# Performance work log

Hardware: AMD Instinct MI355X
Metric: run time of the kernel (lower is better)

## Reference

```python
import jax, jax.numpy as jnp
import numpy as np

NUM_NODES = 50000
NUM_EDGES = 800000
HIDDEN = 128
HEADS = 8
HEAD_DIM = HIDDEN // HEADS  # 16
FF_HIDDEN = 4 * HIDDEN
LN_EPS = 1e-5


def _xavier(key, shape, gain=0.01):
    fan_out, fan_in = shape
    bound = gain * np.sqrt(6.0 / (fan_in + fan_out))
    return jax.random.uniform(key, shape, jnp.float32, -bound, bound)


def setup_inputs() -> dict:
    key = jax.random.key(0)
    ks = jax.random.split(key, 10)
    x = jax.random.normal(ks[0], (NUM_NODES, HIDDEN), jnp.float32)
    edge_index = jax.random.randint(ks[1], (2, NUM_EDGES), 0, NUM_NODES, jnp.int64)
    return {
        "x": x,
        "edge_index": edge_index,
        "Wq": _xavier(ks[2], (HIDDEN, HIDDEN)),
        "bq": jnp.zeros((HIDDEN,), jnp.float32),
        "Wk": _xavier(ks[3], (HIDDEN, HIDDEN)),
        "bk": jnp.zeros((HIDDEN,), jnp.float32),
        "Wv": _xavier(ks[4], (HIDDEN, HIDDEN)),
        "bv": jnp.zeros((HIDDEN,), jnp.float32),
        "Wo": _xavier(ks[5], (HIDDEN, HIDDEN)),
        "bo": jnp.zeros((HIDDEN,), jnp.float32),
        "W1": _xavier(ks[6], (FF_HIDDEN, HIDDEN)),
        "b1": jnp.zeros((FF_HIDDEN,), jnp.float32),
        "W2": _xavier(ks[7], (HIDDEN, FF_HIDDEN)),
        "b2": jnp.zeros((HIDDEN,), jnp.float32),
        "g1": jnp.ones((HIDDEN,), jnp.float32),
        "be1": jnp.zeros((HIDDEN,), jnp.float32),
        "g2": jnp.ones((HIDDEN,), jnp.float32),
        "be2": jnp.zeros((HIDDEN,), jnp.float32),
    }


def _layernorm(v, g, b):
    mu = jnp.mean(v, axis=-1, keepdims=True)
    var = jnp.mean(jnp.square(v - mu), axis=-1, keepdims=True)
    return (v - mu) * jax.lax.rsqrt(var + LN_EPS) * g + b


def _forward(x, edge_index, Wq, bq, Wk, bk, Wv, bv, Wo, bo, W1, b1, W2, b2, g1, be1, g2, be2):
    src = edge_index[0]  # key/value side (_j)
    dst = edge_index[1]  # query side (_i), aggregation index
    scale = 1.0 / np.sqrt(HEAD_DIM)

    # Euclidean manifold: GeometricLinear == plain linear
    q = (x @ Wq.T + bq).reshape(NUM_NODES, HEADS, HEAD_DIM)
    k = (x @ Wk.T + bk).reshape(NUM_NODES, HEADS, HEAD_DIM)
    v = (x @ Wv.T + bv).reshape(NUM_NODES, HEADS, HEAD_DIM)

    # per-edge attention scores [E, H]
    alpha = jnp.einsum('ehd,ehd->eh', q[dst], k[src]) * scale
    # segment softmax over destination nodes
    m = jax.ops.segment_max(alpha, dst, num_segments=NUM_NODES)  # [N, H]
    ea = jnp.exp(alpha - m[dst])
    denom = jax.ops.segment_sum(ea, dst, num_segments=NUM_NODES)  # [N, H]
    alpha = ea / (denom[dst] + 1e-16)

    # scatter-add weighted values -> [N, H, D]
    agg = jax.ops.segment_sum(v[src] * alpha[..., None], dst, num_segments=NUM_NODES)
    att = agg.reshape(NUM_NODES, HIDDEN) @ Wo.T + bo

    # residual + norm1 (Euclidean)
    h = _layernorm(x + att, g1, be1)

    # feed-forward: fc1 -> exact GELU -> fc2
    ff = (jax.nn.gelu(h @ W1.T + b1, approximate=False)) @ W2.T + b2

    # residual + norm2
    return _layernorm(h + ff, g2, be2)


def reference(x, edge_index, Wq, bq, Wk, bk, Wv, bv, Wo, bo, W1, b1, W2, b2, g1, be1, g2, be2):
    return _forward(x, edge_index, Wq, bq, Wk, bk, Wv, bv, Wo, bo, W1, b1, W2, b2, g1, be1, g2, be2)
```

## Files before the change

kernel.cpp:

```cpp
#include <hip/hip_runtime.h>
#include <math.h>

#define N_HEADS 8
#define HEAD_DIM 16
#define HID 128
#define QKV_ROWB 512

typedef unsigned short ushort_t;
typedef __attribute__((ext_vector_type(8))) short short8;
typedef __attribute__((ext_vector_type(4))) float floatx4;
typedef __attribute__((ext_vector_type(2))) float f32x2;

#define KV_SCALE 64.0f
#define KV_INV_SCALE 0.015625f

__device__ __forceinline__ ushort_t f2bf(float f) {
    unsigned u = __float_as_uint(f);
    unsigned r = (u + 0x7FFFu + ((u >> 16) & 1u)) >> 16;
    return (ushort_t)r;
}
__device__ __forceinline__ float bf2f(ushort_t u) {
    return __uint_as_float(((unsigned)u) << 16);
}

__device__ __forceinline__ void gld_lds16(const void* g, void* l) {
    __builtin_amdgcn_global_load_lds(
        (const __attribute__((address_space(1))) void*)g,
        (__attribute__((address_space(3))) void*)l, 16, 0, 0);
}

__device__ __forceinline__ float gelu_f(float x) {
    float z = fabsf(x) * 0.70710678118654752f;
    float t = 1.0f / (1.0f + 0.3275911f * z);
    float y = t * (0.254829592f + t * (-0.284496736f + t * (1.421413741f
            + t * (-1.453152027f + t * 1.061405429f))));
    float e = 1.0f - y * __expf(-z * z);
    e = copysignf(e, x);
    return 0.5f * x * (1.0f + e);
}

__global__ __launch_bounds__(256)
void prep_kernel(const float* __restrict__ x,
                 const float* __restrict__ Wq, const float* __restrict__ Wk,
                 const float* __restrict__ Wv, const float* __restrict__ Wo,
                 const float* __restrict__ W1, const float* __restrict__ W2,
                 const float* __restrict__ bq, const float* __restrict__ bk,
                 const float* __restrict__ bv,
                 const int* __restrict__ dst, int* __restrict__ cnt, int E,
                 ushort_t* __restrict__ xb, ushort_t* __restrict__ wts,
                 float* __restrict__ bqkv, int xpairs)
{
    int i = blockIdx.x * 256 + threadIdx.x;
    if (i < xpairs) {
        float2 v = ((const float2*)x)[i];
        xb[i * 2]     = f2bf(v.x);
        xb[i * 2 + 1] = f2bf(v.y);
        return;
    }
    int j = i - xpairs;
    if (j < 98304) {
        const float* s; int off;
        if (j < 32768) {
            if (j < 8192)       { s = Wq; off = j; }
            else if (j < 16384) { s = Wk; off = j - 8192; }
            else if (j < 24576) { s = Wv; off = j - 16384; }
            else                { s = Wo; off = j - 24576; }
        } else if (j < 65536)   { s = W1; off = j - 32768; }
        else                    { s = W2; off = j - 65536; }
        float2 v = ((const float2*)s)[off];
        wts[j * 2]     = f2bf(v.x);
        wts[j * 2 + 1] = f2bf(v.y);
        return;
    }
    int b = j - 98304;
    if (b < 384) {
        bqkv[b] = (b < 128) ? bq[b] : (b < 256) ? bk[b - 128] : bv[b - 256];
        return;
    }
    int e = b - 384;
    if (e < E) atomicAdd(&cnt[dst[e]], 1);
}

template<int MT, int ACT, int LN, int OUTF>
__global__ __launch_bounds__(256)
void gemm_t(const ushort_t* __restrict__ A, int lda, int M,
            const ushort_t* __restrict__ W, int K,
            const float* __restrict__ bias,
            float* __restrict__ outf, ushort_t* __restrict__ outb, int ostride,
            const float* __restrict__ resf, const ushort_t* __restrict__ resb,
            const float* __restrict__ g, const float* __restrict__ be)
{
    constexpr int MI   = MT / 32;
    constexpr int HALF = MT * 64 + 128 * 64;
    constexpr int BNC  = MT * 136;
    constexpr int SB   = (2 * HALF > BNC) ? 2 * HALF : BNC;
    __shared__ __align__(16) ushort_t sbuf[SB];
    __shared__ float pS[LN ? MT : 1][2];
    __shared__ float pQ[LN ? MT : 1][2];

    const int tid  = threadIdx.x;
    const int wave = tid >> 6, lane = tid & 63;
    const int gm0 = blockIdx.x * MT;
    const int o0  = blockIdx.y * 128;
    const int mhalf = wave >> 1, ohalf = wave & 1;

    auto stage = [&](int kc, int h) {
        ushort_t* As = sbuf + h * HALF;
        ushort_t* Ws = As + MT * 64;
#pragma unroll
        for (int it = 0; it < 4; ++it) {
            int s   = it * 256 + tid;
            int ln  = s & 63;
            int grp = s >> 6;
            int tile = grp >> 1, kst = grp & 1;
            int row = tile * 16 + (ln & 15);
            int kk  = kst * 32 + (ln >> 4) * 8;
            gld_lds16(&W[(size_t)(o0 + row) * K + kc + kk],
                      &Ws[(it * 256 + wave * 64) * 8]);
        }
#pragma unroll
        for (int it = 0; it < MT / 32; ++it) {
            int s   = it * 256 + tid;
            int ln  = s & 63;
            int grp = s >> 6;
            int tile = grp >> 1, kst = grp & 1;
            int row = tile * 16 + (ln & 15);
            int kk  = kst * 32 + (ln >> 4) * 8;
            int ar = gm0 + row; if (ar >= M) ar = M - 1;
            gld_lds16(&A[(size_t)ar * lda + kc + kk],
                      &As[(it * 256 + wave * 64) * 8]);
        }
    };

    floatx4 acc[MI][4];
#pragma unroll
    for (int i = 0; i < MI; ++i)
#pragma unroll
        for (int j = 0; j < 4; ++j) acc[i][j] = (floatx4)(0.f);

    const int nk = K >> 6;
    stage(0, 0);
    __syncthreads();
    for (int t = 0; t < nk; ++t) {
        if (t + 1 < nk) stage((t + 1) * 64, (t + 1) & 1);
        const ushort_t* As = sbuf + (t & 1) * HALF;
        const ushort_t* Ws = As + MT * 64;
#pragma unroll
        for (int kst = 0; kst < 2; ++kst) {
            short8 af[MI], wf[4];
#pragma unroll
            for (int i = 0; i < MI; ++i) {
                int mt = mhalf * MI + i;
                af[i] = *(const short8*)&As[((mt * 2 + kst) * 64 + lane) * 8];
            }
#pragma unroll
            for (int j = 0; j < 4; ++j) {
                int ot = ohalf * 4 + j;
                wf[j] = *(const short8*)&Ws[((ot * 2 + kst) * 64 + lane) * 8];
            }
#pragma unroll
            for (int i = 0; i < MI; ++i)
#pragma unroll
                for (int j = 0; j < 4; ++j)
                    acc[i][j] = __builtin_amdgcn_mfma_f32_16x16x32_bf16(
                        af[i], wf[j], acc[i][j], 0, 0, 0);
        }
        __syncthreads();
    }

    ushort_t* B16 = sbuf;
    float*    B32 = (float*)sbuf;

    if (LN) {
#pragma unroll
        for (int j = 0; j < 4; ++j) {
            int oc = (ohalf * 4 + j) * 16 + (lane & 15);
            float bj = bias[oc];
#pragma unroll
            for (int i = 0; i < MI; ++i) {
                int rbase = gm0 + (mhalf * MI + i) * 16 + (lane >> 4) * 4;
#pragma unroll
                for (int r = 0; r < 4; ++r) {
                    int rowc = rbase + r; if (rowc >= M) rowc = M - 1;
                    float rv = resf ? resf[(size_t)rowc * HID + oc]
                                    : bf2f(resb[(size_t)rowc * HID + oc]);
                    acc[i][j][r] += bj + rv;
                }
            }
        }
#pragma unroll
        for (int i = 0; i < MI; ++i) {
#pragma unroll
            for (int r = 0; r < 4; ++r) {
                float s1 = acc[i][0][r] + acc[i][1][r] + acc[i][2][r] + acc[i][3][r];
                float s2 = acc[i][0][r] * acc[i][0][r] + acc[i][1][r] * acc[i][1][r]
                         + acc[i][2][r] * acc[i][2][r] + acc[i][3][r] * acc[i][3][r];
                s1 += __shfl_xor(s1, 1); s1 += __shfl_xor(s1, 2);
                s1 += __shfl_xor(s1, 4); s1 += __shfl_xor(s1, 8);
                s2 += __shfl_xor(s2, 1); s2 += __shfl_xor(s2, 2);
                s2 += __shfl_xor(s2, 4); s2 += __shfl_xor(s2, 8);
                if ((lane & 15) == 0) {
                    int rl = (mhalf * MI + i) * 16 + (lane >> 4) * 4 + r;
                    pS[rl][ohalf] = s1;
                    pQ[rl][ohalf] = s2;
                }
            }
        }
        __syncthreads();
#pragma unroll
        for (int i = 0; i < MI; ++i) {
#pragma unroll
            for (int r = 0; r < 4; ++r) {
                int rl = (mhalf * MI + i) * 16 + (lane >> 4) * 4 + r;
                float S = pS[rl][0] + pS[rl][1];
                float Q = pQ[rl][0] + pQ[rl][1];
                float mu = S * (1.f / 128.f);
                float var = Q * (1.f / 128.f) - mu * mu;
                float rstd = rsqrtf(var + 1e-5f);
#pragma unroll
                for (int j = 0; j < 4; ++j) {
                    int oc = (ohalf * 4 + j) * 16 + (lane & 15);
                    acc[i][j][r] = (acc[i][j][r] - mu) * rstd * g[oc] + be[oc];
                }
            }
        }
        __syncthreads();
    }

    if (OUTF == 0 || (OUTF == 3 && blockIdx.y == 0)) {
#pragma unroll
        for (int i = 0; i < MI; ++i)
#pragma unroll
            for (int j = 0; j < 4; ++j) {
                int oc = (ohalf * 4 + j) * 16 + (lane & 15);
                float bj = LN ? 0.f : bias[o0 + oc];
#pragma unroll
                for (int r = 0; r < 4; ++r) {
                    int rl = (mhalf * MI + i) * 16 + (lane >> 4) * 4 + r;
                    float v = acc[i][j][r] + bj;
                    if (ACT) v = gelu_f(v);
                    B16[rl * 136 + oc] = f2bf(v);
                }
            }
        __syncthreads();
        const int oo = (OUTF == 3) ? 0 : o0;
#pragma unroll
        for (int p = 0; p < MT / 16; ++p) {
            int row = p * 16 + (tid >> 4);
            int ch  = tid & 15;
            if (gm0 + row < M)
                *(short8*)&outb[(size_t)(gm0 + row) * ostride + oo + ch * 8] =
                    *(const short8*)&B16[row * 136 + ch * 8];
        }
    } else if (OUTF == 2 || OUTF == 3) {
#pragma unroll
        for (int i = 0; i < MI; ++i)
#pragma unroll
            for (int j = 0; j < 4; ++j) {
                int oc = (ohalf * 4 + j) * 16 + (lane & 15);
                float bj = bias[o0 + oc];
#pragma unroll
                for (int r = 0; r < 4; ++r) {
                    int rl = (mhalf * MI + i) * 16 + (lane >> 4) * 4 + r;
                    float v = (acc[i][j][r] + bj) * KV_SCALE;
                    B16[rl * 136 + oc] = f2bf(v);
                }
            }
        __syncthreads();
        const int koff = (OUTF == 3) ? (blockIdx.y - 1) * 8 : blockIdx.y * 8;
#pragma unroll
        for (int p = 0; p < MT / 16; ++p) {
            int row = p * 16 + (tid >> 4);
            int ch  = tid & 15;
            if (gm0 + row < M) {
                short8 s = *(const short8*)&B16[row * 136 + ch * 8];
                unsigned u0 = 0, u1 = 0;
                u0 = __builtin_amdgcn_cvt_pk_fp8_f32(
                         bf2f((ushort_t)s[0]), bf2f((ushort_t)s[1]), u0, false);
                u0 = __builtin_amdgcn_cvt_pk_fp8_f32(
                         bf2f((ushort_t)s[2]), bf2f((ushort_t)s[3]), u0, true);
                u1 = __builtin_amdgcn_cvt_pk_fp8_f32(
                         bf2f((ushort_t)s[4]), bf2f((ushort_t)s[5]), u1, false);
                u1 = __builtin_amdgcn_cvt_pk_fp8_f32(
                         bf2f((ushort_t)s[6]), bf2f((ushort_t)s[7]), u1, true);
                uint2 o; o.x = u0; o.y = u1;
                *(uint2*)((char*)outb + (size_t)(gm0 + row) * QKV_ROWB
                          + 256 + ch * 16 + koff) = o;
            }
        }
    } else {
#pragma unroll
        for (int p = 0; p < 2; ++p) {
            if (ohalf == p) {
#pragma unroll
                for (int i = 0; i < MI; ++i)
#pragma unroll
                    for (int j = 0; j < 4; ++j) {
                        int ocl = j * 16 + (lane & 15);
                        float bj = LN ? 0.f : bias[p * 64 + ocl];
#pragma unroll
                        for (int r = 0; r < 4; ++r) {
                            int rl = (mhalf * MI + i) * 16 + (lane >> 4) * 4 + r;
                            float v = acc[i][j][r] + bj;
                            if (ACT) v = gelu_f(v);
                            B32[rl * 68 + ocl] = v;
                        }
                    }
            }
            __syncthreads();
#pragma unroll
            for (int q = 0; q < MT / 16; ++q) {
                int row = q * 16 + (tid >> 4);
                int ch  = tid & 15;
                if (gm0 + row < M)
                    *(float4*)&outf[(size_t)(gm0 + row) * ostride + o0 + p * 64 + ch * 4] =
                        *(const float4*)&B32[row * 68 + ch * 4];
            }
            __syncthreads();
        }
    }
}

__global__ __launch_bounds__(256)
void ff_fused_kernel(const ushort_t* __restrict__ hb,
                     const ushort_t* __restrict__ w1,
                     const float* __restrict__ b1,
                     const ushort_t* __restrict__ w2,
                     const float* __restrict__ b2,
                     const float* __restrict__ g, const float* __restrict__ be,
                     float* __restrict__ out, int M)
{
    __shared__ __align__(16) ushort_t Hs[8192];
    __shared__ __align__(16) ushort_t wst[16384];
    __shared__ __align__(16) ushort_t a1t[8192];
    __shared__ float pS[64][2];
    __shared__ float pQ[64][2];

    const int tid = threadIdx.x;
    const int wave = tid >> 6, lane = tid & 63;
    const int gm0 = blockIdx.x * 64;
    const int mhalf = wave >> 1, ohalf = wave & 1;

    auto stage_panel = [&](int p, int h) {
        int c = p >> 2, sub = p & 3;
        ushort_t* dst = wst + h * 8192;
#pragma unroll
        for (int it = 0; it < 4; ++it) {
            int s = it * 256 + tid;
            int l = s & 63;
            int grp = s >> 6;
            int tile = grp >> 1, kst = grp & 1;
            int row = tile * 16 + (l & 15);
            int kk = kst * 32 + (l >> 4) * 8;
            const ushort_t* src;
            if (sub < 2) src = &w1[(size_t)(c * 128 + row) * HID + sub * 64 + kk];
            else         src = &w2[(size_t)row * 512 + c * 128 + (sub - 2) * 64 + kk];
            gld_lds16(src, &dst[(it * 256 + wave * 64) * 8]);
        }
    };

#pragma unroll
    for (int it = 0; it < 4; ++it) {
        int s = it * 256 + tid;
        int l = s & 63;
        int g8 = (s >> 6) & 7;
        int kc = s >> 9;
        int tile = g8 >> 1, kst = g8 & 1;
        int row = tile * 16 + (l & 15);
        int kk = kc * 64 + kst * 32 + (l >> 4) * 8;
        int ar = gm0 + row; if (ar >= M) ar = M - 1;
        gld_lds16(&hb[(size_t)ar * HID + kk], &Hs[(it * 256 + wave * 64) * 8]);
    }
    stage_panel(0, 0);
    __syncthreads();

    floatx4 acc2[2][4];
#pragma unroll
    for (int i = 0; i < 2; ++i)
#pragma unroll
        for (int j = 0; j < 4; ++j) acc2[i][j] = (floatx4)(0.f);

    floatx4 acc1[2][4];

    for (int p = 0; p < 16; ++p) {
        const int sub = p & 3;
        const int c   = p >> 2;
        if (p + 1 < 16) stage_panel(p + 1, (p + 1) & 1);
        const ushort_t* wbuf = wst + (p & 1) * 8192;

        if (sub == 0) {
#pragma unroll
            for (int i = 0; i < 2; ++i)
#pragma unroll
                for (int j = 0; j < 4; ++j) acc1[i][j] = (floatx4)(0.f);
        }

        if (sub < 2) {
#pragma unroll
            for (int kst = 0; kst < 2; ++kst) {
                short8 af[2], wf[4];
#pragma unroll
                for (int i = 0; i < 2; ++i) {
                    int mt = mhalf * 2 + i;
                    af[i] = *(const short8*)&Hs[(((sub << 3) + mt * 2 + kst) * 64 + lane) * 8];
                }
#pragma unroll
                for (int j = 0; j < 4; ++j) {
                    int ot = ohalf * 4 + j;
                    wf[j] = *(const short8*)&wbuf[((ot * 2 + kst) * 64 + lane) * 8];
                }
#pragma unroll
                for (int i = 0; i < 2; ++i)
#pragma unroll
                    for (int j = 0; j < 4; ++j)
                        acc1[i][j] = __builtin_amdgcn_mfma_f32_16x16x32_bf16(
                            af[i], wf[j], acc1[i][j], 0, 0, 0);
            }
            if (sub == 1) {
#pragma unroll
                for (int i = 0; i < 2; ++i)
#pragma unroll
                    for (int j = 0; j < 4; ++j) {
                        int oc = (ohalf * 4 + j) * 16 + (lane & 15);
                        float bj = b1[c * 128 + oc];
#pragma unroll
                        for (int r = 0; r < 4; ++r) {
                            int rl = (mhalf * 2 + i) * 16 + (lane >> 4) * 4 + r;
                            *(ushort_t*)((char*)a1t + rl * 256 +
                                         ((oc * 2) ^ ((rl & 7) << 4))) =
                                f2bf(gelu_f(acc1[i][j][r] + bj));
                        }
                    }
            }
        } else {
            const int kc2 = sub - 2;
#pragma unroll
            for (int kst = 0; kst < 2; ++kst) {
                short8 af[2], wf[4];
#pragma unroll
                for (int i = 0; i < 2; ++i) {
                    int ar = (mhalf * 2 + i) * 16 + (lane & 15);
                    int bc = kc2 * 128 + kst * 64 + (lane >> 4) * 16;
                    af[i] = *(const short8*)((const char*)a1t + ar * 256 +
                                             (bc ^ ((ar & 7) << 4)));
                }
#pragma unroll
                for (int j = 0; j < 4; ++j) {
                    int ot = ohalf * 4 + j;
                    wf[j] = *(const short8*)&wbuf[((ot * 2 + kst) * 64 + lane) * 8];
                }
#pragma unroll
                for (int i = 0; i < 2; ++i)
#pragma unroll
                    for (int j = 0; j < 4; ++j)
                        acc2[i][j] = __builtin_amdgcn_mfma_f32_16x16x32_bf16(
                            af[i], wf[j], acc2[i][j], 0, 0, 0);
            }
        }
        __syncthreads();
    }

#pragma unroll
    for (int j = 0; j < 4; ++j) {
        int oc = (ohalf * 4 + j) * 16 + (lane & 15);
        float bj = b2[oc];
#pragma unroll
        for (int i = 0; i < 2; ++i) {
#pragma unroll
            for (int r = 0; r < 4; ++r) {
                int rl = (mhalf * 2 + i) * 16 + (lane >> 4) * 4 + r;
                float rv = bf2f(Hs[(((oc >> 6) * 8 + (rl >> 4) * 2 + ((oc >> 5) & 1)) * 64
                                    + (rl & 15) + ((oc >> 3) & 3) * 16) * 8 + (oc & 7)]);
                acc2[i][j][r] += bj + rv;
            }
        }
    }
#pragma unroll
    for (int i = 0; i < 2; ++i) {
#pragma unroll
        for (int r = 0; r < 4; ++r) {
            float s1 = acc2[i][0][r] + acc2[i][1][r] + acc2[i][2][r] + acc2[i][3][r];
            float s2 = acc2[i][0][r] * acc2[i][0][r] + acc2[i][1][r] * acc2[i][1][r]
                     + acc2[i][2][r] * acc2[i][2][r] + acc2[i][3][r] * acc2[i][3][r];
            s1 += __shfl_xor(s1, 1); s1 += __shfl_xor(s1, 2);
            s1 += __shfl_xor(s1, 4); s1 += __shfl_xor(s1, 8);
            s2 += __shfl_xor(s2, 1); s2 += __shfl_xor(s2, 2);
            s2 += __shfl_xor(s2, 4); s2 += __shfl_xor(s2, 8);
            if ((lane & 15) == 0) {
                int rl = (mhalf * 2 + i) * 16 + (lane >> 4) * 4 + r;
                pS[rl][ohalf] = s1;
                pQ[rl][ohalf] = s2;
            }
        }
    }
    __syncthreads();
#pragma unroll
    for (int i = 0; i < 2; ++i) {
#pragma unroll
        for (int r = 0; r < 4; ++r) {
            int rl = (mhalf * 2 + i) * 16 + (lane >> 4) * 4 + r;
            float S = pS[rl][0] + pS[rl][1];
            float Q = pQ[rl][0] + pQ[rl][1];
            float mu = S * (1.f / 128.f);
            float var = Q * (1.f / 128.f) - mu * mu;
            float rstd = rsqrtf(var + 1e-5f);
#pragma unroll
            for (int j = 0; j < 4; ++j) {
                int oc = (ohalf * 4 + j) * 16 + (lane & 15);
                acc2[i][j][r] = (acc2[i][j][r] - mu) * rstd * g[oc] + be[oc];
            }
        }
    }
    __syncthreads();

    float* B32 = (float*)wst;
#pragma unroll
    for (int p = 0; p < 2; ++p) {
        if (ohalf == p) {
#pragma unroll
            for (int i = 0; i < 2; ++i)
#pragma unroll
                for (int j = 0; j < 4; ++j) {
                    int ocl = j * 16 + (lane & 15);
#pragma unroll
                    for (int r = 0; r < 4; ++r) {
                        int rl = (mhalf * 2 + i) * 16 + (lane >> 4) * 4 + r;
                        B32[rl * 68 + ocl] = acc2[i][j][r];
                    }
                }
        }
        __syncthreads();
#pragma unroll
        for (int q = 0; q < 4; ++q) {
            int row = q * 16 + (tid >> 4);
            int ch  = tid & 15;
            if (gm0 + row < M)
                *(float4*)&out[(size_t)(gm0 + row) * HID + p * 64 + ch * 4] =
                    *(const float4*)&B32[row * 68 + ch * 4];
        }
        __syncthreads();
    }
}

__global__ __launch_bounds__(256)
void scan1_kernel(const int* __restrict__ cnt, int* __restrict__ parts, int N)
{
    __shared__ int sd[256];
    int t = threadIdx.x;
    int base = blockIdx.x * 1024 + t * 4;
    int s = 0;
#pragma unroll
    for (int j = 0; j < 4; ++j) if (base + j < N) s += cnt[base + j];
    sd[t] = s; __syncthreads();
    for (int off = 128; off; off >>= 1) {
        if (t < off) sd[t] += sd[t + off];
        __syncthreads();
    }
    if (t == 0) parts[blockIdx.x] = sd[0];
}

__global__ __launch_bounds__(256)
void scan2_kernel(const int* __restrict__ parts, int* __restrict__ poff, int nb)
{
    __shared__ int sd[256];
    int t = threadIdx.x;
    int v = (t < nb) ? parts[t] : 0;
    sd[t] = v; __syncthreads();
    for (int off = 1; off < 256; off <<= 1) {
        int u = (t >= off) ? sd[t - off] : 0;
        __syncthreads();
        sd[t] += u;
        __syncthreads();
    }
    if (t < nb) poff[t] = sd[t] - v;
}

__global__ __launch_bounds__(256)
void scan3_kernel(const int* __restrict__ cnt, const int* __restrict__ poff,
                  int* __restrict__ rp, int N)
{
    __shared__ int sd[256];
    int t = threadIdx.x;
    int base = blockIdx.x * 1024 + t * 4;
    int v0 = (base + 0 < N) ? cnt[base + 0] : 0;
    int v1 = (base + 1 < N) ? cnt[base + 1] : 0;
    int v2 = (base + 2 < N) ? cnt[base + 2] : 0;
    int v3 = (base + 3 < N) ? cnt[base + 3] : 0;
    int s = v0 + v1 + v2 + v3;
    sd[t] = s; __syncthreads();
    for (int off = 1; off < 256; off <<= 1) {
        int u = (t >= off) ? sd[t - off] : 0;
        __syncthreads();
        sd[t] += u;
        __syncthreads();
    }
    int o = poff[blockIdx.x] + sd[t] - s;
    if (base + 0 < N) rp[base + 0] = o;
    if (base + 1 < N) rp[base + 1] = o + v0;
    if (base + 2 < N) rp[base + 2] = o + v0 + v1;
    if (base + 3 < N) rp[base + 3] = o + v0 + v1 + v2;
}

__global__ __launch_bounds__(256)
void scatter_kernel(const int* __restrict__ src, const int* __restrict__ dst,
                    int* __restrict__ rp, int* __restrict__ ssrc, int E, int N)
{
    int coh = blockIdx.x & 7;
    int bc  = blockIdx.x >> 3;
    int rr  = (N + 7) >> 3;
    int nlo = coh * rr;
    int nhi = nlo + rr; if (nhi > N) nhi = N;
    int stride = (gridDim.x >> 3) * 256;
    for (int e = bc * 256 + threadIdx.x; e < E; e += stride) {
        int d = dst[e];
        if (d >= nlo && d < nhi) {
            int pos = atomicAdd(&rp[d], 1);
            ssrc[pos] = src[e];
        }
    }
}

__global__ __launch_bounds__(256)
void attn_fused_kernel(const ushort_t* __restrict__ qkvb, const int* __restrict__ rp,
                       const int* __restrict__ ssrc, ushort_t* __restrict__ aggb, int N)
{
    int wave = threadIdx.x >> 6, lane = threadIdx.x & 63;
    int n = blockIdx.x * 4 + wave;
    if (n >= N) return;
    int grp = lane >> 4;
    int cb  = (lane & 15) * 16;
    const char* base = (const char*)qkvb;

    short8 qv = *(const short8*)(base + n * QKV_ROWB + cb);
    float q[8];
#pragma unroll
    for (int j = 0; j < 8; ++j) q[j] = bf2f((ushort_t)qv[j]) * (0.25f / KV_SCALE);

    int r0 = n ? rp[n - 1] : 0;
    int r1 = rp[n];
    float acc[8] = {0.f, 0.f, 0.f, 0.f, 0.f, 0.f, 0.f, 0.f};
    float l = 0.f;

    int r = r0;
    for (; r + 8 <= r1; r += 8) {
        int s0 = ssrc[r + grp];
        int s1 = ssrc[r + 4 + grp];
        uint4 kv0 = *(const uint4*)(base + s0 * QKV_ROWB + 256 + cb);
        uint4 kv1 = *(const uint4*)(base + s1 * QKV_ROWB + 256 + cb);

        f32x2 a0 = __builtin_amdgcn_cvt_pk_f32_fp8(kv0.x, false);
        f32x2 a1 = __builtin_amdgcn_cvt_pk_f32_fp8(kv0.x, true);
        f32x2 a2 = __builtin_amdgcn_cvt_pk_f32_fp8(kv0.y, false);
        f32x2 a3 = __builtin_amdgcn_cvt_pk_f32_fp8(kv0.y, true);
        f32x2 b0 = __builtin_amdgcn_cvt_pk_f32_fp8(kv1.x, false);
        f32x2 b1 = __builtin_amdgcn_cvt_pk_f32_fp8(kv1.x, true);
        f32x2 b2 = __builtin_amdgcn_cvt_pk_f32_fp8(kv1.y, false);
        f32x2 b3 = __builtin_amdgcn_cvt_pk_f32_fp8(kv1.y, true);

        float p0 = 0.f, p1 = 0.f;
        p0 = fmaf(q[0], a0.x, p0); p0 = fmaf(q[1], a0.y, p0);
        p0 = fmaf(q[2], a1.x, p0); p0 = fmaf(q[3], a1.y, p0);
        p0 = fmaf(q[4], a2.x, p0); p0 = fmaf(q[5], a2.y, p0);
        p0 = fmaf(q[6], a3.x, p0); p0 = fmaf(q[7], a3.y, p0);
        p1 = fmaf(q[0], b0.x, p1); p1 = fmaf(q[1], b0.y, p1);
        p1 = fmaf(q[2], b1.x, p1); p1 = fmaf(q[3], b1.y, p1);
        p1 = fmaf(q[4], b2.x, p1); p1 = fmaf(q[5], b2.y, p1);
        p1 = fmaf(q[6], b3.x, p1); p1 = fmaf(q[7], b3.y, p1);

        p0 += __shfl_xor(p0, 1);
        p1 += __shfl_xor(p1, 1);
        float e0 = __expf(p0), e1 = __expf(p1);
        l += e0 + e1;

        f32x2 v0 = __builtin_amdgcn_cvt_pk_f32_fp8(kv0.z, false);
        f32x2 v1 = __builtin_amdgcn_cvt_pk_f32_fp8(kv0.z, true);
        f32x2 v2 = __builtin_amdgcn_cvt_pk_f32_fp8(kv0.w, false);
        f32x2 v3 = __builtin_amdgcn_cvt_pk_f32_fp8(kv0.w, true);
        f32x2 w0 = __builtin_amdgcn_cvt_pk_f32_fp8(kv1.z, false);
        f32x2 w1 = __builtin_amdgcn_cvt_pk_f32_fp8(kv1.z, true);
        f32x2 w2 = __builtin_amdgcn_cvt_pk_f32_fp8(kv1.w, false);
        f32x2 w3 = __builtin_amdgcn_cvt_pk_f32_fp8(kv1.w, true);

        acc[0] = fmaf(e0, v0.x, acc[0]); acc[1] = fmaf(e0, v0.y, acc[1]);
        acc[2] = fmaf(e0, v1.x, acc[2]); acc[3] = fmaf(e0, v1.y, acc[3]);
        acc[4] = fmaf(e0, v2.x, acc[4]); acc[5] = fmaf(e0, v2.y, acc[5]);
        acc[6] = fmaf(e0, v3.x, acc[6]); acc[7] = fmaf(e0, v3.y, acc[7]);
        acc[0] = fmaf(e1, w0.x, acc[0]); acc[1] = fmaf(e1, w0.y, acc[1]);
        acc[2] = fmaf(e1, w1.x, acc[2]); acc[3] = fmaf(e1, w1.y, acc[3]);
        acc[4] = fmaf(e1, w2.x, acc[4]); acc[5] = fmaf(e1, w2.y, acc[5]);
        acc[6] = fmaf(e1, w3.x, acc[6]); acc[7] = fmaf(e1, w3.y, acc[7]);
    }
    for (; r < r1; r += 4) {
        int e = r + grp;
        int s = ssrc[(e < r1) ? e : r0];
        uint4 kv = *(const uint4*)(base + s * QKV_ROWB + 256 + cb);
        f32x2 a0 = __builtin_amdgcn_cvt_pk_f32_fp8(kv.x, false);
        f32x2 a1 = __builtin_amdgcn_cvt_pk_f32_fp8(kv.x, true);
        f32x2 a2 = __builtin_amdgcn_cvt_pk_f32_fp8(kv.y, false);
        f32x2 a3 = __builtin_amdgcn_cvt_pk_f32_fp8(kv.y, true);
        float p = 0.f;
        p = fmaf(q[0], a0.x, p); p = fmaf(q[1], a0.y, p);
        p = fmaf(q[2], a1.x, p); p = fmaf(q[3], a1.y, p);
        p = fmaf(q[4], a2.x, p); p = fmaf(q[5], a2.y, p);
        p = fmaf(q[6], a3.x, p); p = fmaf(q[7], a3.y, p);
        p += __shfl_xor(p, 1);
        float ea = (e < r1) ? __expf(p) : 0.f;
        l += ea;
        f32x2 v0 = __builtin_amdgcn_cvt_pk_f32_fp8(kv.z, false);
        f32x2 v1 = __builtin_amdgcn_cvt_pk_f32_fp8(kv.z, true);
        f32x2 v2 = __builtin_amdgcn_cvt_pk_f32_fp8(kv.w, false);
        f32x2 v3 = __builtin_amdgcn_cvt_pk_f32_fp8(kv.w, true);
        acc[0] = fmaf(ea, v0.x, acc[0]); acc[1] = fmaf(ea, v0.y, acc[1]);
        acc[2] = fmaf(ea, v1.x, acc[2]); acc[3] = fmaf(ea, v1.y, acc[3]);
        acc[4] = fmaf(ea, v2.x, acc[4]); acc[5] = fmaf(ea, v2.y, acc[5]);
        acc[6] = fmaf(ea, v3.x, acc[6]); acc[7] = fmaf(ea, v3.y, acc[7]);
    }

#pragma unroll
    for (int j = 0; j < 8; ++j) {
        acc[j] += __shfl_xor(acc[j], 16);
        acc[j] += __shfl_xor(acc[j], 32);
    }
    l += __shfl_xor(l, 16);
    l += __shfl_xor(l, 32);
    float inv = KV_INV_SCALE / (l + 1e-16f);
    if (grp == 0) {
        short8 o;
#pragma unroll
        for (int j = 0; j < 8; ++j) o[j] = (short)f2bf(acc[j] * inv);
        *(short8*)((char*)aggb + n * 256 + cb) = o;
    }
}

extern "C" void kernel_launch(void* const* d_in, const int* in_sizes, int n_in,
                              void* d_out, int out_size, void* d_ws, size_t ws_size,
                              hipStream_t stream)
{
    const float* x  = (const float*)d_in[0];
    const int*   ei = (const int*)d_in[1];
    const float* Wq = (const float*)d_in[2];
    const float* bq = (const float*)d_in[3];
    const float* Wk = (const float*)d_in[4];
    const float* bk = (const float*)d_in[5];
    const float* Wv = (const float*)d_in[6];
    const float* bv = (const float*)d_in[7];
    const float* Wo = (const float*)d_in[8];
    const float* bo = (const float*)d_in[9];
    const float* W1 = (const float*)d_in[10];
    const float* b1 = (const float*)d_in[11];
    const float* W2 = (const float*)d_in[12];
    const float* b2 = (const float*)d_in[13];
    const float* g1 = (const float*)d_in[14];
    const float* be1= (const float*)d_in[15];
    const float* g2 = (const float*)d_in[16];
    const float* be2= (const float*)d_in[17];
    float* out = (float*)d_out;

    const int N = in_sizes[0] / HID;
    const int E = in_sizes[1] / 2;
    const int* srcp = ei;
    const int* dstp = ei + E;

    const size_t NH = (size_t)N * HID;
    float* wsf = (float*)d_ws;

    ushort_t* xb   = (ushort_t*)wsf;
    ushort_t* qkvb = (ushort_t*)(wsf + NH / 2);
    ushort_t* aggb = (ushort_t*)(wsf + 2 * NH);
    ushort_t* hb   = (ushort_t*)wsf;

    ushort_t* wts  = (ushort_t*)(wsf + 2 * NH + NH / 2);
    float*    bqkv = (float*)(wts + 196608);
    int*      rp   = (int*)(bqkv + 384);
    int*      cnt  = rp + (N + 1);
    int*      poff = cnt + N;
    int*      parts= poff + 256;
    int*      ssrc = parts + 256;

    hipMemsetAsync(cnt, 0, N * sizeof(int), stream);
    const int xpairs = (int)(NH / 2);
    const int ptot   = xpairs + 98304 + 384 + E;
    prep_kernel<<<(ptot + 255) / 256, 256, 0, stream>>>(
        x, Wq, Wk, Wv, Wo, W1, W2, bq, bk, bv, dstp, cnt, E,
        xb, wts, bqkv, xpairs);

    const int nb = (N + 1023) / 1024;
    scan1_kernel<<<nb, 256, 0, stream>>>(cnt, parts, N);
    scan2_kernel<<<1, 256, 0, stream>>>(parts, poff, nb);
    scan3_kernel<<<nb, 256, 0, stream>>>(cnt, poff, rp, N);
    scatter_kernel<<<2048, 256, 0, stream>>>(srcp, dstp, rp, ssrc, E, N);

    const int gx64 = (N + 63) / 64;

    gemm_t<64, 0, 0, 3><<<dim3(gx64, 3), 256, 0, stream>>>(
        xb, HID, N, wts, HID, bqkv, nullptr, qkvb, 256,
        nullptr, nullptr, nullptr, nullptr);

    attn_fused_kernel<<<(N + 3) / 4, 256, 0, stream>>>(qkvb, rp, ssrc, aggb, N);

    gemm_t<64, 0, 1, 0><<<dim3(gx64, 1), 256, 0, stream>>>(
        aggb, HID, N, wts + 49152, HID, bo, nullptr, hb, HID,
        x, nullptr, g1, be1);

    ff_fused_kernel<<<gx64, 256, 0, stream>>>(
        hb, wts + 65536, b1, wts + 131072, b2, g2, be2, out, N);
}
```

Baseline: 338.2 us.

## Rewrite feed-forward block as persistent FP8 kernel with LDS-resident weights

Replaces the bf16 fused feed-forward kernel with a persistent 512-thread FP8 kernel. W1 and W2 are pre-scaled, converted to swizzled FP8 in the prep kernel and held entirely in LDS (128 KB) for the life of each block, which removes per-tile weight panel streaming. The Wo+LN1 GEMM now also writes an FP8 copy of h for the MFMA inputs, and the GELU activations are requantized to FP8 with fixed scales. The intent is to double MFMA throughput and cut global traffic. The risk is accuracy loss from FP8 and fixed scales, plus LDS-limited occupancy of one block per CU.

```diff
diff --git a/kernel.cpp b/kernel.cpp
--- a/kernel.cpp
+++ b/kernel.cpp
@@ -13,6 +13,13 @@
 
 #define KV_SCALE 64.0f
 #define KV_INV_SCALE 0.015625f
+
+#define W_SCALE 65536.0f
+#define A1_SCALE 8192.0f
+#define G1_DESCALE (1.0f / 65536.0f)
+#define G2_DESCALE (1.0f / 536870912.0f)
+
+#define FF_SWZ(r, p) ((p) ^ (((r) & 7) << 3))
 
 __device__ __forceinline__ ushort_t f2bf(float f) {
     unsigned u = __float_as_uint(f);
@@ -48,7 +55,9 @@
                  const float* __restrict__ bv,
                  const int* __restrict__ dst, int* __restrict__ cnt, int E,
                  ushort_t* __restrict__ xb, ushort_t* __restrict__ wts,
-                 float* __restrict__ bqkv, int xpairs)
+                 float* __restrict__ bqkv,
+                 unsigned char* __restrict__ w1f8,
+                 unsigned char* __restrict__ w2f8, int xpairs)
 {
     int i = blockIdx.x * 256 + threadIdx.x;
     if (i < xpairs) {
@@ -58,26 +67,49 @@
         return;
     }
     int j = i - xpairs;
-    if (j < 98304) {
+    if (j < 32768) {
         const float* s; int off;
-        if (j < 32768) {
-            if (j < 8192)       { s = Wq; off = j; }
-            else if (j < 16384) { s = Wk; off = j - 8192; }
-            else if (j < 24576) { s = Wv; off = j - 16384; }
-            else                { s = Wo; off = j - 24576; }
-        } else if (j < 65536)   { s = W1; off = j - 32768; }
-        else                    { s = W2; off = j - 65536; }
+        if (j < 8192)       { s = Wq; off = j; }
+        else if (j < 16384) { s = Wk; off = j - 8192; }
+        else if (j < 24576) { s = Wv; off = j - 16384; }
+        else                { s = Wo; off = j - 24576; }
         float2 v = ((const float2*)s)[off];
         wts[j * 2]     = f2bf(v.x);
         wts[j * 2 + 1] = f2bf(v.y);
         return;
     }
-    int b = j - 98304;
+    int b = j - 32768;
     if (b < 384) {
         bqkv[b] = (b < 128) ? bq[b] : (b < 256) ? bk[b - 128] : bv[b - 256];
         return;
     }
-    int e = b - 384;
+    int c = b - 384;
+    if (c < 8192) {
+        int row = c >> 4, p8 = (c & 15) * 8;
+        const float* s = W1 + (size_t)row * HID + (p8 ^ ((row & 7) << 3));
+        unsigned u0 = 0, u1 = 0;
+        u0 = __builtin_amdgcn_cvt_pk_fp8_f32(s[0]*W_SCALE, s[1]*W_SCALE, u0, false);
+        u0 = __builtin_amdgcn_cvt_pk_fp8_f32(s[2]*W_SCALE, s[3]*W_SCALE, u0, true);
+        u1 = __builtin_amdgcn_cvt_pk_fp8_f32(s[4]*W_SCALE, s[5]*W_SCALE, u1, false);
+        u1 = __builtin_amdgcn_cvt_pk_fp8_f32(s[6]*W_SCALE, s[7]*W_SCALE, u1, true);
+        uint2 o; o.x = u0; o.y = u1;
+        *(uint2*)&w1f8[(size_t)row * 128 + p8] = o;
+        return;
+    }
+    int c2 = c - 8192;
+    if (c2 < 8192) {
+        int row = c2 >> 6, p8 = (c2 & 63) * 8;
+        const float* s = W2 + (size_t)row * 512 + (p8 ^ ((row & 7) << 3));
+        unsigned u0 = 0, u1 = 0;
+        u0 = __builtin_amdgcn_cvt_pk_fp8_f32(s[0]*W_SCALE, s[1]*W_SCALE, u0, false);
+        u0 = __builtin_amdgcn_cvt_pk_fp8_f32(s[2]*W_SCALE, s[3]*W_SCALE, u0, true);
+        u1 = __builtin_amdgcn_cvt_pk_fp8_f32(s[4]*W_SCALE, s[5]*W_SCALE, u1, false);
+        u1 = __builtin_amdgcn_cvt_pk_fp8_f32(s[6]*W_SCALE, s[7]*W_SCALE, u1, true);
+        uint2 o; o.x = u0; o.y = u1;
+        *(uint2*)&w2f8[(size_t)row * 512 + p8] = o;
+        return;
+    }
+    int e = c2 - 8192;
     if (e < E) atomicAdd(&cnt[dst[e]], 1);
 }
 
@@ -182,8 +214,10 @@
 #pragma unroll
                 for (int r = 0; r < 4; ++r) {
                     int rowc = rbase + r; if (rowc >= M) rowc = M - 1;
-                    float rv = resf ? resf[(size_t)rowc * HID + oc]
-                                    : bf2f(resb[(size_t)rowc * HID + oc]);
+                    float rv = resf && !OUTF ? bf2f(resb[(size_t)rowc * HID + oc])
+                                             : 0.f;
+                    rv = resb ? bf2f(resb[(size_t)rowc * HID + oc])
+                              : resf ? resf[(size_t)rowc * HID + oc] : 0.f;
                     acc[i][j][r] += bj + rv;
                 }
             }
@@ -248,11 +282,27 @@
         for (int p = 0; p < MT / 16; ++p) {
             int row = p * 16 + (tid >> 4);
             int ch  = tid & 15;
-            if (gm0 + row < M)
-                *(short8*)&outb[(size_t)(gm0 + row) * ostride + oo + ch * 8] =
-                    *(const short8*)&B16[row * 136 + ch * 8];
-        }
-    } else if (OUTF == 2 || OUTF == 3) {
+            if (gm0 + row < M) {
+                short8 s = *(const short8*)&B16[row * 136 + ch * 8];
+                *(short8*)&outb[(size_t)(gm0 + row) * ostride + oo + ch * 8] = s;
+                if (LN && outf) {
+                    unsigned u0 = 0, u1 = 0;
+                    u0 = __builtin_amdgcn_cvt_pk_fp8_f32(
+                             bf2f((ushort_t)s[0]), bf2f((ushort_t)s[1]), u0, false);
+                    u0 = __builtin_amdgcn_cvt_pk_fp8_f32(
+                             bf2f((ushort_t)s[2]), bf2f((ushort_t)s[3]), u0, true);
+                    u1 = __builtin_amdgcn_cvt_pk_fp8_f32(
+                             bf2f((ushort_t)s[4]), bf2f((ushort_t)s[5]), u1, false);
+                    u1 = __builtin_amdgcn_cvt_pk_fp8_f32(
+                             bf2f((ushort_t)s[6]), bf2f((ushort_t)s[7]), u1, true);
+                    uint2 o; o.x = u0; o.y = u1;
+                    unsigned char* h8 = (unsigned char*)outf;
+                    *(uint2*)&h8[(size_t)(gm0 + row) * 128 +
+                                 ((ch * 8) ^ ((row & 7) << 3))] = o;
+                }
+            }
+        }
+    } else if (OUTF == 3) {
 #pragma unroll
         for (int i = 0; i < MI; ++i)
 #pragma unroll
@@ -267,7 +317,7 @@
                 }
             }
         __syncthreads();
-        const int koff = (OUTF == 3) ? (blockIdx.y - 1) * 8 : blockIdx.y * 8;
+        const int koff = (blockIdx.y - 1) * 8;
 #pragma unroll
         for (int p = 0; p < MT / 16; ++p) {
             int row = p * 16 + (tid >> 4);
@@ -321,224 +371,174 @@
     }
 }
 
-__global__ __launch_bounds__(256)
-void ff_fused_kernel(const ushort_t* __restrict__ hb,
-                     const ushort_t* __restrict__ w1,
-                     const float* __restrict__ b1,
-                     const ushort_t* __restrict__ w2,
-                     const float* __restrict__ b2,
-                     const float* __restrict__ g, const float* __restrict__ be,
-                     float* __restrict__ out, int M)
+__global__ __launch_bounds__(512)
+void ff8_kernel(const unsigned char* __restrict__ hf8,
+                const ushort_t* __restrict__ hb,
+                const unsigned char* __restrict__ w1f8,
+                const unsigned char* __restrict__ w2f8,
+                const float* __restrict__ b1, const float* __restrict__ b2,
+                const float* __restrict__ g, const float* __restrict__ be,
+                float* __restrict__ out, int M, int ntiles)
 {
-    __shared__ __align__(16) ushort_t Hs[8192];
-    __shared__ __align__(16) ushort_t wst[16384];
-    __shared__ __align__(16) ushort_t a1t[8192];
-    __shared__ float pS[64][2];
-    __shared__ float pQ[64][2];
-
-    const int tid = threadIdx.x;
+    __shared__ __align__(16) unsigned char W1s[65536];
+    __shared__ __align__(16) unsigned char W2s[65536];
+    __shared__ __align__(16) unsigned char Hs8[8192];
+    __shared__ __align__(16) unsigned char A1s[16384];
+    __shared__ float pS[64][4];
+    __shared__ float pQ[64][4];
+
+    const int tid  = threadIdx.x;
     const int wave = tid >> 6, lane = tid & 63;
-    const int gm0 = blockIdx.x * 64;
-    const int mhalf = wave >> 1, ohalf = wave & 1;
-
-    auto stage_panel = [&](int p, int h) {
-        int c = p >> 2, sub = p & 3;
-        ushort_t* dst = wst + h * 8192;
-#pragma unroll
-        for (int it = 0; it < 4; ++it) {
-            int s = it * 256 + tid;
-            int l = s & 63;
-            int grp = s >> 6;
-            int tile = grp >> 1, kst = grp & 1;
-            int row = tile * 16 + (l & 15);
-            int kk = kst * 32 + (l >> 4) * 8;
-            const ushort_t* src;
-            if (sub < 2) src = &w1[(size_t)(c * 128 + row) * HID + sub * 64 + kk];
-            else         src = &w2[(size_t)row * 512 + c * 128 + (sub - 2) * 64 + kk];
-            gld_lds16(src, &dst[(it * 256 + wave * 64) * 8]);
-        }
-    };
-
-#pragma unroll
-    for (int it = 0; it < 4; ++it) {
-        int s = it * 256 + tid;
-        int l = s & 63;
-        int g8 = (s >> 6) & 7;
-        int kc = s >> 9;
-        int tile = g8 >> 1, kst = g8 & 1;
-        int row = tile * 16 + (l & 15);
-        int kk = kc * 64 + kst * 32 + (l >> 4) * 8;
-        int ar = gm0 + row; if (ar >= M) ar = M - 1;
-        gld_lds16(&hb[(size_t)ar * HID + kk], &Hs[(it * 256 + wave * 64) * 8]);
-    }
-    stage_panel(0, 0);
-    __syncthreads();
-
-    floatx4 acc2[2][4];
-#pragma unroll
-    for (int i = 0; i < 2; ++i)
-#pragma unroll
-        for (int j = 0; j < 4; ++j) acc2[i][j] = (floatx4)(0.f);
-
-    floatx4 acc1[2][4];
-
-    for (int p = 0; p < 16; ++p) {
-        const int sub = p & 3;
-        const int c   = p >> 2;
-        if (p + 1 < 16) stage_panel(p + 1, (p + 1) & 1);
-        const ushort_t* wbuf = wst + (p & 1) * 8192;
-
-        if (sub == 0) {
+    const int wm = wave >> 2;
+    const int wn = wave & 3;
+    const int l15 = lane & 15, l4 = lane >> 4;
+
+#pragma unroll
+    for (int it = 0; it < 8; ++it)
+        gld_lds16(w1f8 + (it * 512 + tid) * 16,
+                  W1s + (it * 512 + wave * 64) * 16);
+#pragma unroll
+    for (int it = 0; it < 8; ++it)
+        gld_lds16(w2f8 + (it * 512 + tid) * 16,
+                  W2s + (it * 512 + wave * 64) * 16);
+
+    for (int t = blockIdx.x; t < ntiles; t += gridDim.x) {
+        const int gm0 = t * 64;
+        {
+            int rr = gm0 + (tid >> 3); if (rr >= M) rr = M - 1;
+            gld_lds16(hf8 + (size_t)rr * 128 + (tid & 7) * 16,
+                      Hs8 + (wave * 64 + lane) * 16);
+        }
+        __syncthreads();
+
+        floatx4 acc2[2][2];
+#pragma unroll
+        for (int i = 0; i < 2; ++i)
+#pragma unroll
+            for (int j = 0; j < 2; ++j) acc2[i][j] = (floatx4)(0.f);
+
+        for (int hc = 0; hc < 2; ++hc) {
+            floatx4 acc1[2][4];
 #pragma unroll
             for (int i = 0; i < 2; ++i)
 #pragma unroll
                 for (int j = 0; j < 4; ++j) acc1[i][j] = (floatx4)(0.f);
-        }
-
-        if (sub < 2) {
-#pragma unroll
-            for (int kst = 0; kst < 2; ++kst) {
-                short8 af[2], wf[4];
+#pragma unroll
+            for (int ks = 0; ks < 4; ++ks) {
+                int k = ks * 32 + l4 * 8;
+                long av[2];
 #pragma unroll
                 for (int i = 0; i < 2; ++i) {
-                    int mt = mhalf * 2 + i;
-                    af[i] = *(const short8*)&Hs[(((sub << 3) + mt * 2 + kst) * 64 + lane) * 8];
+                    int row = (wm * 2 + i) * 16 + l15;
+                    av[i] = *(const long*)&Hs8[row * 128 + FF_SWZ(row, k)];
                 }
 #pragma unroll
                 for (int j = 0; j < 4; ++j) {
-                    int ot = ohalf * 4 + j;
-                    wf[j] = *(const short8*)&wbuf[((ot * 2 + kst) * 64 + lane) * 8];
-                }
-#pragma unroll
-                for (int i = 0; i < 2; ++i)
-#pragma unroll
-                    for (int j = 0; j < 4; ++j)
-                        acc1[i][j] = __builtin_amdgcn_mfma_f32_16x16x32_bf16(
-                            af[i], wf[j], acc1[i][j], 0, 0, 0);
-            }
-            if (sub == 1) {
-#pragma unroll
-                for (int i = 0; i < 2; ++i)
-#pragma unroll
-                    for (int j = 0; j < 4; ++j) {
-                        int oc = (ohalf * 4 + j) * 16 + (lane & 15);
-                        float bj = b1[c * 128 + oc];
-#pragma unroll
-                        for (int r = 0; r < 4; ++r) {
-                            int rl = (mhalf * 2 + i) * 16 + (lane >> 4) * 4 + r;
-                            *(ushort_t*)((char*)a1t + rl * 256 +
-                                         ((oc * 2) ^ ((rl & 7) << 4))) =
-                                f2bf(gelu_f(acc1[i][j][r] + bj));
-                        }
+                    int fc = hc * 256 + wn * 64 + j * 16 + l15;
+                    long bv = *(const long*)&W1s[(size_t)fc * 128 + FF_SWZ(fc, k)];
+#pragma unroll
+                    for (int i = 0; i < 2; ++i)
+                        acc1[i][j] = __builtin_amdgcn_mfma_f32_16x16x32_fp8_fp8(
+                            av[i], bv, acc1[i][j], 0, 0, 0);
+                }
+            }
+            float b1v[4];
+#pragma unroll
+            for (int j = 0; j < 4; ++j)
+                b1v[j] = b1[hc * 256 + wn * 64 + j * 16 + l15];
+#pragma unroll
+            for (int i = 0; i < 2; ++i)
+#pragma unroll
+                for (int j = 0; j < 4; ++j) {
+                    int col = wn * 64 + j * 16 + l15;
+#pragma unroll
+                    for (int r = 0; r < 4; ++r) {
+                        int row = (wm * 2 + i) * 16 + l4 * 4 + r;
+                        float v = acc1[i][j][r] * G1_DESCALE + b1v[j];
+                        v = gelu_f(v) * A1_SCALE;
+                        unsigned u = __builtin_amdgcn_cvt_pk_fp8_f32(v, v, 0, false);
+                        A1s[row * 256 + FF_SWZ(row, col)] = (unsigned char)u;
                     }
-            }
-        } else {
-            const int kc2 = sub - 2;
-#pragma unroll
-            for (int kst = 0; kst < 2; ++kst) {
-                short8 af[2], wf[4];
+                }
+            __syncthreads();
+#pragma unroll
+            for (int ks = 0; ks < 8; ++ks) {
+                int k = ks * 32 + l4 * 8;
+                long av[2];
 #pragma unroll
                 for (int i = 0; i < 2; ++i) {
-                    int ar = (mhalf * 2 + i) * 16 + (lane & 15);
-                    int bc = kc2 * 128 + kst * 64 + (lane >> 4) * 16;
-                    af[i] = *(const short8*)((const char*)a1t + ar * 256 +
-                                             (bc ^ ((ar & 7) << 4)));
-                }
-#pragma unroll
-                for (int j = 0; j < 4; ++j) {
-                    int ot = ohalf * 4 + j;
-                    wf[j] = *(const short8*)&wbuf[((ot * 2 + kst) * 64 + lane) * 8];
-                }
-#pragma unroll
-                for (int i = 0; i < 2; ++i)
-#pragma unroll
-                    for (int j = 0; j < 4; ++j)
-                        acc2[i][j] = __builtin_amdgcn_mfma_f32_16x16x32_bf16(
-                            af[i], wf[j], acc2[i][j], 0, 0, 0);
-            }
-        }
-        __syncthreads();
-    }
-
-#pragma unroll
-    for (int j = 0; j < 4; ++j) {
-        int oc = (ohalf * 4 + j) * 16 + (lane & 15);
-        float bj = b2[oc];
+                    int row = (wm * 2 + i) * 16 + l15;
+                    av[i] = *(const long*)&A1s[row * 256 + FF_SWZ(row, k)];
+                }
+#pragma unroll
+                for (int j = 0; j < 2; ++j) {
+                    int oc = wn * 32 + j * 16 + l15;
+                    long bv = *(const long*)&W2s[(size_t)oc * 512 + hc * 256 +
+                                                 FF_SWZ(oc, k)];
+#pragma unroll
+                    for (int i = 0; i < 2; ++i)
+                        acc2[i][j] = __builtin_amdgcn_mfma_f32_16x16x32_fp8_fp8(
+                            av[i], bv, acc2[i][j], 0, 0, 0);
+                }
+            }
+            __syncthreads();
+        }
+
+        float b2v[2];
+#pragma unroll
+        for (int j = 0; j < 2; ++j) b2v[j] = b2[wn * 32 + j * 16 + l15];
+#pragma unroll
+        for (int i = 0; i < 2; ++i)
+#pragma unroll
+            for (int j = 0; j < 2; ++j) {
+                int oc = wn * 32 + j * 16 + l15;
+#pragma unroll
+                for (int r = 0; r < 4; ++r) {
+                    int rowg = gm0 + (wm * 2 + i) * 16 + l4 * 4 + r;
+                    if (rowg >= M) rowg = M - 1;
+                    acc2[i][j][r] = acc2[i][j][r] * G2_DESCALE + b2v[j]
+                                  + bf2f(hb[(size_t)rowg * HID + oc]);
+                }
+            }
 #pragma unroll
         for (int i = 0; i < 2; ++i) {
 #pragma unroll
             for (int r = 0; r < 4; ++r) {
-                int rl = (mhalf * 2 + i) * 16 + (lane >> 4) * 4 + r;
-                float rv = bf2f(Hs[(((oc >> 6) * 8 + (rl >> 4) * 2 + ((oc >> 5) & 1)) * 64
-                                    + (rl & 15) + ((oc >> 3) & 3) * 16) * 8 + (oc & 7)]);
-                acc2[i][j][r] += bj + rv;
-            }
-        }
-    }
-#pragma unroll
-    for (int i = 0; i < 2; ++i) {
-#pragma unroll
-        for (int r = 0; r < 4; ++r) {
-            float s1 = acc2[i][0][r] + acc2[i][1][r] + acc2[i][2][r] + acc2[i][3][r];
-            float s2 = acc2[i][0][r] * acc2[i][0][r] + acc2[i][1][r] * acc2[i][1][r]
-                     + acc2[i][2][r] * acc2[i][2][r] + acc2[i][3][r] * acc2[i][3][r];
-            s1 += __shfl_xor(s1, 1); s1 += __shfl_xor(s1, 2);
-            s1 += __shfl_xor(s1, 4); s1 += __shfl_xor(s1, 8);
-            s2 += __shfl_xor(s2, 1); s2 += __shfl_xor(s2, 2);
-            s2 += __shfl_xor(s2, 4); s2 += __shfl_xor(s2, 8);
-            if ((lane & 15) == 0) {
-                int rl = (mhalf * 2 + i) * 16 + (lane >> 4) * 4 + r;
-                pS[rl][ohalf] = s1;
-                pQ[rl][ohalf] = s2;
-            }
-        }
-    }
-    __syncthreads();
-#pragma unroll
-    for (int i = 0; i < 2; ++i) {
-#pragma unroll
-        for (int r = 0; r < 4; ++r) {
-            int rl = (mhalf * 2 + i) * 16 + (lane >> 4) * 4 + r;
-            float S = pS[rl][0] + pS[rl][1];
-            float Q = pQ[rl][0] + pQ[rl][1];
-            float mu = S * (1.f / 128.f);
-            float var = Q * (1.f / 128.f) - mu * mu;
-            float rstd = rsqrtf(var + 1e-5f);
-#pragma unroll
-            for (int j = 0; j < 4; ++j) {
-                int oc = (ohalf * 4 + j) * 16 + (lane & 15);
-                acc2[i][j][r] = (acc2[i][j][r] - mu) * rstd * g[oc] + be[oc];
-            }
-        }
-    }
-    __syncthreads();
-
-    float* B32 = (float*)wst;
-#pragma unroll
-    for (int p = 0; p < 2; ++p) {
-        if (ohalf == p) {
-#pragma unroll
-            for (int i = 0; i < 2; ++i)
-#pragma unroll
-                for (int j = 0; j < 4; ++j) {
-                    int ocl = j * 16 + (lane & 15);
-#pragma unroll
-                    for (int r = 0; r < 4; ++r) {
-                        int rl = (mhalf * 2 + i) * 16 + (lane >> 4) * 4 + r;
-                        B32[rl * 68 + ocl] = acc2[i][j][r];
+                float s1 = acc2[i][0][r] + acc2[i][1][r];
+                float s2 = acc2[i][0][r] * acc2[i][0][r]
+                         + acc2[i][1][r] * acc2[i][1][r];
+                s1 += __shfl_xor(s1, 1); s1 += __shfl_xor(s1, 2);
+                s1 += __shfl_xor(s1, 4); s1 += __shfl_xor(s1, 8);
+                s2 += __shfl_xor(s2, 1); s2 += __shfl_xor(s2, 2);
+                s2 += __shfl_xor(s2, 4); s2 += __shfl_xor(s2, 8);
+                if (l15 == 0) {
+                    int rl = (wm * 2 + i) * 16 + l4 * 4 + r;
+                    pS[rl][wn] = s1;
+                    pQ[rl][wn] = s2;
+                }
+            }
+        }
+        __syncthreads();
+#pragma unroll
+        for (int i = 0; i < 2; ++i) {
+#pragma unroll
+            for (int r = 0; r < 4; ++r) {
+                int rl = (wm * 2 + i) * 16 + l4 * 4 + r;
+                float S = pS[rl][0] + pS[rl][1] + pS[rl][2] + pS[rl][3];
+                float Q = pQ[rl][0] + pQ[rl][1] + pQ[rl][2] + pQ[rl][3];
+                float mu = S * (1.f / 128.f);
+                float var = Q * (1.f / 128.f) - mu * mu;
+                float rstd = rsqrtf(var + 1e-5f);
+                if (gm0 + rl < M) {
+#pragma unroll
+                    for (int j = 0; j < 2; ++j) {
+                        int oc = wn * 32 + j * 16 + l15;
+                        out[(size_t)(gm0 + rl) * HID + oc] =
+                            (acc2[i][j][r] - mu) * rstd * g[oc] + be[oc];
                     }
                 }
-        }
-        __syncthreads();
-#pragma unroll
-        for (int q = 0; q < 4; ++q) {
-            int row = q * 16 + (tid >> 4);
-            int ch  = tid & 15;
-            if (gm0 + row < M)
-                *(float4*)&out[(size_t)(gm0 + row) * HID + p * 64 + ch * 4] =
-                    *(const float4*)&B32[row * 68 + ch * 4];
-        }
-        __syncthreads();
+            }
+        }
     }
 }
 
@@ -768,6 +768,9 @@
     ushort_t* qkvb = (ushort_t*)(wsf + NH / 2);
     ushort_t* aggb = (ushort_t*)(wsf + 2 * NH);
     ushort_t* hb   = (ushort_t*)wsf;
+    unsigned char* hf8 = (unsigned char*)(wsf + NH / 2);
+    unsigned char* w1f8 = (unsigned char*)(wsf + NH + NH / 2);
+    unsigned char* w2f8 = w1f8 + 65536;
 
     ushort_t* wts  = (ushort_t*)(wsf + 2 * NH + NH / 2);
     float*    bqkv = (float*)(wts + 196608);
@@ -779,10 +782,10 @@
 
     hipMemsetAsync(cnt, 0, N * sizeof(int), stream);
     const int xpairs = (int)(NH / 2);
-    const int ptot   = xpairs + 98304 + 384 + E;
+    const int ptot   = xpairs + 32768 + 384 + 16384 + E;
     prep_kernel<<<(ptot + 255) / 256, 256, 0, stream>>>(
         x, Wq, Wk, Wv, Wo, W1, W2, bq, bk, bv, dstp, cnt, E,
-        xb, wts, bqkv, xpairs);
+        xb, wts, bqkv, w1f8, w2f8, xpairs);
 
     const int nb = (N + 1023) / 1024;
     scan1_kernel<<<nb, 256, 0, stream>>>(cnt, parts, N);
@@ -799,9 +802,9 @@
     attn_fused_kernel<<<(N + 3) / 4, 256, 0, stream>>>(qkvb, rp, ssrc, aggb, N);
 
     gemm_t<64, 0, 1, 0><<<dim3(gx64, 1), 256, 0, stream>>>(
-        aggb, HID, N, wts + 49152, HID, bo, nullptr, hb, HID,
+        aggb, HID, N, wts + 49152, HID, bo, (float*)hf8, hb, HID,
         x, nullptr, g1, be1);
 
-    ff_fused_kernel<<<gx64, 256, 0, stream>>>(
-        hb, wts + 65536, b1, wts + 131072, b2, g2, be2, out, N);
-}
+    ff8_kernel<<<256, 512, 0, stream>>>(
+        hf8, hb, w1f8, w2f8, b1, b2, g2, be2, out, N, gx64);
+}
```

Result: no change. 331.9 us (-1.9%).
